# Performance work log

Hardware: AMD Instinct MI355X
Metric: run time of the kernel (lower is better)

## Reference

```python
import jax, jax.numpy as jnp
import numpy as np

N = 100_000      # total nodes across batch of graphs
E = 1_600_000    # total directed edges
D = 128          # input feature dim
H = 128          # hidden dim
OUT = 10         # output classes
B = 500          # number of graphs (200 nodes each)
L_MID = 3        # GIN layers after the first (num_layers-2)


def setup_inputs() -> dict:
    key = jax.random.key(0)
    ks = jax.random.split(key, 24)
    s = np.float32(1.0 / np.sqrt(H))
    f32 = jnp.float32
    inp = {
        'node_features': jax.random.normal(ks[0], (N, D), f32),
        'edge_src': jax.random.randint(ks[1], (E,), 0, N, jnp.int32),
        'edge_dst': jax.random.randint(ks[2], (E,), 0, N, jnp.int32),
        'graph_ids': (jnp.arange(N) // (N // B)).astype(jnp.int32),
        # GIN eps per layer (torch init: zeros)
        'eps': jnp.zeros((4,), f32),
        # pre MLP (input layer): Linear(D,H) -> BN -> ReLU -> Linear(H,H), then pre_batchnorm
        'pre_W1': jax.random.normal(ks[3], (D, H), f32) * s,
        'pre_b1': jnp.zeros((H,), f32),
        'pre_g1': jnp.ones((H,), f32),
        'pre_bt1': jnp.zeros((H,), f32),
        'pre_W2': jax.random.normal(ks[4], (H, H), f32) * s,
        'pre_b2': jnp.zeros((H,), f32),
        'pre_gout': jnp.ones((H,), f32),
        'pre_btout': jnp.zeros((H,), f32),
        # middle GIN layers (stacked over L_MID)
        'mlp_W1': jax.random.normal(ks[5], (L_MID, H, H), f32) * s,
        'mlp_b1': jnp.zeros((L_MID, H), f32),
        'mlp_g1': jnp.ones((L_MID, H), f32),
        'mlp_bt1': jnp.zeros((L_MID, H), f32),
        'mlp_W2': jax.random.normal(ks[6], (L_MID, H, H), f32) * s,
        'mlp_b2': jnp.zeros((L_MID, H), f32),
        'bn_g': jnp.ones((L_MID, H), f32),
        'bn_bt': jnp.zeros((L_MID, H), f32),
        # per-layer prediction heads
        'pred_W0': jax.random.normal(ks[7], (D, OUT), f32) * s,
        'pred_b0': jnp.zeros((OUT,), f32),
        'pred_W': jax.random.normal(ks[8], (4, H, OUT), f32) * s,
        'pred_b': jnp.zeros((4, OUT), f32),
    }
    return inp


def _mlp_bn(x, W1, b1, g1, bt1, W2, b2, go, bo):
    # MLP(num_mlp_layers=2): Linear -> BN(eval) -> ReLU -> Linear, then outer BN(eval) -> ReLU
    h = jax.nn.relu(g1 * (x @ W1 + b1) + bt1)
    h = h @ W2 + b2
    return jax.nn.relu(go * h + bo)


def reference(node_features, edge_src, edge_dst, graph_ids, eps,
              pre_W1, pre_b1, pre_g1, pre_bt1, pre_W2, pre_b2, pre_gout, pre_btout,
              mlp_W1, mlp_b1, mlp_g1, mlp_bt1, mlp_W2, mlp_b2, bn_g, bn_bt,
              pred_W0, pred_b0, pred_W, pred_b):
    def agg(h):
        # sparse Adj @ h via gather + segment_sum (sum neighbor pooling, learn_eps=True -> no self loops)
        return jax.ops.segment_sum(h[edge_src], edge_dst, num_segments=N)

    h = node_features
    reps = [h]
    pooled = agg(h) + (1.0 + eps[0]) * h
    h = _mlp_bn(pooled, pre_W1, pre_b1, pre_g1, pre_bt1, pre_W2, pre_b2, pre_gout, pre_btout)
    reps.append(h)
    for i in range(L_MID):
        pooled = agg(h) + (1.0 + eps[i + 1]) * h
        h = _mlp_bn(pooled, mlp_W1[i], mlp_b1[i], mlp_g1[i], mlp_bt1[i],
                    mlp_W2[i], mlp_b2[i], bn_g[i], bn_bt[i])
        reps.append(h)

    # graph-level sum pooling + per-layer linear heads (dropout off in eval)
    score = jax.ops.segment_sum(reps[0], graph_ids, num_segments=B) @ pred_W0 + pred_b0
    for k in range(4):
        score = score + jax.ops.segment_sum(reps[k + 1], graph_ids, num_segments=B) @ pred_W[k] + pred_b[k]
    return score  # [B, OUT]
```

## Files before the change

### kernel.cpp

```cpp
#include <hip/hip_runtime.h>
#include <hip/hip_bf16.h>

#define NN 100000
#define EE 1600000
#define HH 128
#define OUTC 10
#define BB 500
#define GSZ 200
#define LDA 136

#define NBKT 782
#define BCAP 2560
#define EPB 4096

typedef float f32x4 __attribute__((ext_vector_type(4)));
typedef __bf16 bf16x8 __attribute__((ext_vector_type(8)));

__device__ __forceinline__ float b2f(unsigned short u){
    unsigned int x = ((unsigned int)u) << 16;
    return __builtin_bit_cast(float, x);
}
__device__ __forceinline__ unsigned short f2b(float f){
    __hip_bfloat16 h = __float2bfloat16(f);
    return __builtin_bit_cast(unsigned short, h);
}

__global__ __launch_bounds__(256) void k_bucket(const int* __restrict__ src, const int* __restrict__ dst,
                                                int* __restrict__ bucket_cursor, unsigned int* __restrict__ ebuf){
    __shared__ unsigned int val[EPB];
    __shared__ unsigned short bkt[EPB];
    __shared__ int hist[NBKT];
    int t = threadIdx.x;
    int e0 = blockIdx.x * EPB;
    for (int i = t; i < NBKT; i += 256) hist[i] = 0;
    __syncthreads();
    for (int i = t; i < EPB; i += 256){
        int e = e0 + i;
        if (e < EE){
            int d = dst[e];
            int b = d >> 7;
            val[i] = ((unsigned)src[e] << 7) | (unsigned)(d & 127);
            bkt[i] = (unsigned short)b;
            atomicAdd(&hist[b], 1);
        } else {
            bkt[i] = 0xffff;
        }
    }
    __syncthreads();
    for (int i = t; i < NBKT; i += 256){
        int c = hist[i];
        hist[i] = c ? atomicAdd(&bucket_cursor[i], c) : 0;
    }
    __syncthreads();
    for (int i = t; i < EPB; i += 256){
        unsigned short b = bkt[i];
        if (b != 0xffff){
            int pos = atomicAdd(&hist[b], 1);
            if (pos < BCAP) ebuf[(int)b * BCAP + pos] = val[i];
        }
    }
}

__global__ __launch_bounds__(1024) void k_bscan(const int* __restrict__ bucket_cursor,
                                                int* __restrict__ bucket_base, int* __restrict__ row_ptr){
    __shared__ int tmp[1024];
    int t = threadIdx.x;
    int v = (t < NBKT) ? min(bucket_cursor[t], BCAP) : 0;
    tmp[t] = v; __syncthreads();
    for (int off = 1; off < 1024; off <<= 1){
        int a = (t >= off) ? tmp[t - off] : 0;
        __syncthreads();
        tmp[t] += a;
        __syncthreads();
    }
    if (t < NBKT) bucket_base[t + 1] = tmp[t];
    if (t == 0){ bucket_base[0] = 0; row_ptr[NN] = EE; }
}

__global__ __launch_bounds__(256) void k_csr(const int* __restrict__ bucket_cursor, const int* __restrict__ bucket_base,
                                             const unsigned int* __restrict__ ebuf,
                                             int* __restrict__ row_ptr, int* __restrict__ col){
    __shared__ int cnt[128];
    __shared__ int pfx[128];
    int b = blockIdx.x;
    int t = threadIdx.x;
    int c    = min(bucket_cursor[b], BCAP);
    int base = bucket_base[b];
    if (t < 128) cnt[t] = 0;
    __syncthreads();
    const unsigned int* eb = ebuf + (size_t)b * BCAP;
    for (int i = t; i < c; i += 256) atomicAdd(&cnt[eb[i] & 127], 1);
    __syncthreads();
    if (t == 0){
        int run = 0;
        for (int i = 0; i < 128; ++i){ pfx[i] = run; run += cnt[i]; }
    }
    __syncthreads();
    int node0 = b * 128;
    if (t < 128 && node0 + t < NN) row_ptr[node0 + t] = base + pfx[t];
    if (t < 128) cnt[t] = pfx[t];
    __syncthreads();
    for (int i = t; i < c; i += 256){
        unsigned int v = eb[i];
        int pos = atomicAdd(&cnt[v & 127], 1);
        col[base + pos] = (int)(v >> 7);
    }
}

__global__ __launch_bounds__(256) void k_cast(const float* __restrict__ in, unsigned short* __restrict__ out, int n){
    int i = (blockIdx.x*256 + threadIdx.x)*4;
    if (i < n){
        float4 v = *(const float4*)(in + i);
        uint2 o;
        o.x = (unsigned)f2b(v.x) | ((unsigned)f2b(v.y) << 16);
        o.y = (unsigned)f2b(v.z) | ((unsigned)f2b(v.w) << 16);
        *(uint2*)(out + i) = o;
    }
}

__global__ __launch_bounds__(256) void k_prep(const float* __restrict__ preW1, const float* __restrict__ preW2,
                                              const float* __restrict__ mlpW1, const float* __restrict__ mlpW2,
                                              unsigned short* __restrict__ Wbf){
    int idx = blockIdx.x*256 + threadIdx.x;
    int w = idx >> 14;
    int n = (idx >> 7) & 127;
    int k = idx & 127;
    const float* src;
    if      (w == 0) src = preW1;
    else if (w == 1) src = preW2;
    else if (w <  5) src = mlpW1 + (w-2)*16384;
    else             src = mlpW2 + (w-5)*16384;
    Wbf[idx] = f2b(src[k*128 + n]);
}

__device__ __forceinline__ void acc_u32(float* a, unsigned int v, int j){
    a[j]   += __builtin_bit_cast(float, v << 16);
    a[j+1] += __builtin_bit_cast(float, v & 0xffff0000u);
}
__device__ __forceinline__ void acc_u4(float* a, uint4 v){
    acc_u32(a, v.x, 0); acc_u32(a, v.y, 2); acc_u32(a, v.z, 4); acc_u32(a, v.w, 6);
}

__global__ __launch_bounds__(256) void k_agg(const int* __restrict__ row_ptr, const int* __restrict__ col,
                                             const unsigned short* __restrict__ h,
                                             const float* __restrict__ eps, int l,
                                             unsigned short* __restrict__ pooled){
    int lane = threadIdx.x & 63;
    int wv   = threadIdx.x >> 6;
    int n    = blockIdx.x*4 + wv;
    int q = lane >> 4;
    int u = lane & 15;
    int beg = row_ptr[n], end = row_ptr[n+1];
    float a[8];
    #pragma unroll
    for (int j = 0; j < 8; ++j) a[j] = 0.f;

    int e = beg;
    for (; e + 16 <= end; e += 16){
        int c0 = col[e      + q];
        int c1 = col[e + 4  + q];
        int c2 = col[e + 8  + q];
        int c3 = col[e + 12 + q];
        uint4 v0 = *(const uint4*)(h + (size_t)c0*128 + u*8);
        uint4 v1 = *(const uint4*)(h + (size_t)c1*128 + u*8);
        uint4 v2 = *(const uint4*)(h + (size_t)c2*128 + u*8);
        uint4 v3 = *(const uint4*)(h + (size_t)c3*128 + u*8);
        acc_u4(a, v0); acc_u4(a, v1); acc_u4(a, v2); acc_u4(a, v3);
    }
    for (; e + 4 <= end; e += 4){
        int c = col[e + q];
        uint4 v = *(const uint4*)(h + (size_t)c*128 + u*8);
        acc_u4(a, v);
    }
    if (e < end){
        if (e + q < end){
            int c = col[e + q];
            uint4 v = *(const uint4*)(h + (size_t)c*128 + u*8);
            acc_u4(a, v);
        }
    }
    #pragma unroll
    for (int j = 0; j < 8; ++j){
        a[j] += __shfl_xor(a[j], 16, 64);
        a[j] += __shfl_xor(a[j], 32, 64);
    }
    if (q == 0){
        float ep = 1.0f + eps[l];
        uint4 hs = *(const uint4*)(h + (size_t)n*128 + u*8);
        a[0] += ep * __builtin_bit_cast(float, hs.x << 16);
        a[1] += ep * __builtin_bit_cast(float, hs.x & 0xffff0000u);
        a[2] += ep * __builtin_bit_cast(float, hs.y << 16);
        a[3] += ep * __builtin_bit_cast(float, hs.y & 0xffff0000u);
        a[4] += ep * __builtin_bit_cast(float, hs.z << 16);
        a[5] += ep * __builtin_bit_cast(float, hs.z & 0xffff0000u);
        a[6] += ep * __builtin_bit_cast(float, hs.w << 16);
        a[7] += ep * __builtin_bit_cast(float, hs.w & 0xffff0000u);
        uint4 o;
        o.x = (unsigned)f2b(a[0]) | ((unsigned)f2b(a[1]) << 16);
        o.y = (unsigned)f2b(a[2]) | ((unsigned)f2b(a[3]) << 16);
        o.z = (unsigned)f2b(a[4]) | ((unsigned)f2b(a[5]) << 16);
        o.w = (unsigned)f2b(a[6]) | ((unsigned)f2b(a[7]) << 16);
        *(uint4*)(pooled + (size_t)n*128 + u*8) = o;
    }
}

__global__ __launch_bounds__(256) void k_mlp(const unsigned short* __restrict__ Ain,
                                             unsigned short* __restrict__ Out,
                                             const unsigned short* __restrict__ W1t,
                                             const unsigned short* __restrict__ W2t,
                                             const float* __restrict__ b1, const float* __restrict__ g1,
                                             const float* __restrict__ bt1,
                                             const float* __restrict__ b2, const float* __restrict__ g2,
                                             const float* __restrict__ bt2,
                                             float* __restrict__ Gout){
    __shared__ __align__(16) unsigned short As[64*LDA];
    __shared__ __align__(16) unsigned short Ws[128*LDA];
    int t = threadIdx.x;
    int row0 = blockIdx.x * 64;

    for (int i = t; i < 64*16; i += 256){
        int r = i >> 4, c = i & 15;
        int node = row0 + r;
        int4 v = (node < NN) ? *(const int4*)(Ain + node*128 + c*8) : make_int4(0,0,0,0);
        *(int4*)(&As[r*LDA + c*8]) = v;
    }
    for (int i = t; i < 128*16; i += 256){
        int r = i >> 4, c = i & 15;
        *(int4*)(&Ws[r*LDA + c*8]) = *(const int4*)(W1t + r*128 + c*8);
    }
    __syncthreads();

    int lane = t & 63;
    int wv = t >> 6;
    int rowbase = wv * 16;
    int m = lane & 15, q = lane >> 4;

    f32x4 acc[8];
    #pragma unroll
    for (int j = 0; j < 8; ++j) acc[j] = (f32x4){0.f,0.f,0.f,0.f};
    #pragma unroll
    for (int kk = 0; kk < 4; ++kk){
        bf16x8 a = *(const bf16x8*)(&As[(rowbase + m)*LDA + kk*32 + q*8]);
        #pragma unroll
        for (int j = 0; j < 8; ++j){
            bf16x8 b = *(const bf16x8*)(&Ws[(j*16 + m)*LDA + kk*32 + q*8]);
            acc[j] = __builtin_amdgcn_mfma_f32_16x16x32_bf16(a, b, acc[j], 0, 0, 0);
        }
    }
    #pragma unroll
    for (int j = 0; j < 8; ++j){
        int colc = j*16 + m;
        float bv = b1[colc], gv = g1[colc], btv = bt1[colc];
        #pragma unroll
        for (int r = 0; r < 4; ++r){
            float v = (acc[j][r] + bv)*gv + btv;
            v = fmaxf(v, 0.f);
            As[(rowbase + q*4 + r)*LDA + colc] = f2b(v);
        }
    }
    __syncthreads();
    for (int i = t; i < 128*16; i += 256){
        int r = i >> 4, c = i & 15;
        *(int4*)(&Ws[r*LDA + c*8]) = *(const int4*)(W2t + r*128 + c*8);
    }
    __syncthreads();

    #pragma unroll
    for (int j = 0; j < 8; ++j) acc[j] = (f32x4){0.f,0.f,0.f,0.f};
    #pragma unroll
    for (int kk = 0; kk < 4; ++kk){
        bf16x8 a = *(const bf16x8*)(&As[(rowbase + m)*LDA + kk*32 + q*8]);
        #pragma unroll
        for (int j = 0; j < 8; ++j){
            bf16x8 b = *(const bf16x8*)(&Ws[(j*16 + m)*LDA + kk*32 + q*8]);
            acc[j] = __builtin_amdgcn_mfma_f32_16x16x32_bf16(a, b, acc[j], 0, 0, 0);
        }
    }
    #pragma unroll
    for (int j = 0; j < 8; ++j){
        int colc = j*16 + m;
        float bv = b2[colc], gv = g2[colc], btv = bt2[colc];
        #pragma unroll
        for (int r = 0; r < 4; ++r){
            float v = (acc[j][r] + bv)*gv + btv;
            v = fmaxf(v, 0.f);
            As[(rowbase + q*4 + r)*LDA + colc] = f2b(v);
        }
    }
    __syncthreads();
    for (int i = t; i < 64*16; i += 256){
        int r = i >> 4, c = i & 15;
        int node = row0 + r;
        if (node < NN)
            *(int4*)(Out + node*128 + c*8) = *(const int4*)(&As[r*LDA + c*8]);
    }
    {
        int f = t & 127;
        int rbeg = (t >> 7) * 32;
        float run = 0.f;
        int curg = (row0 + rbeg) / GSZ;
        for (int r = rbeg; r < rbeg + 32; ++r){
            int node = row0 + r;
            if (node >= NN) break;
            int g = node / GSZ;
            if (g != curg){
                if (run != 0.f) atomicAdd(&Gout[curg*128 + f], run);
                run = 0.f; curg = g;
            }
            run += b2f(As[r*LDA + f]);
        }
        if (run != 0.f) atomicAdd(&Gout[curg*128 + f], run);
    }
}

__global__ __launch_bounds__(256) void k_gpool0(const float* __restrict__ h, float* __restrict__ G){
    __shared__ float r0[256], r1[256];
    int t = threadIdx.x;
    int c2 = t & 63, rg = t >> 6;
    int gb = blockIdx.x;
    const float2* h2 = (const float2*)h;
    float a0 = 0.f, a1 = 0.f;
    for (int i = rg; i < GSZ; i += 4){
        float2 v = h2[(gb*GSZ + i)*64 + c2];
        a0 += v.x; a1 += v.y;
    }
    r0[t] = a0; r1[t] = a1;
    __syncthreads();
    if (t < 64){
        float s0 = r0[t] + r0[t+64] + r0[t+128] + r0[t+192];
        float s1 = r1[t] + r1[t+64] + r1[t+128] + r1[t+192];
        float2 v; v.x = s0; v.y = s1;
        *(float2*)(G + gb*128 + t*2) = v;
    }
}

__global__ __launch_bounds__(256) void k_score(const float* __restrict__ G,
                                               const float* __restrict__ W0, const float* __restrict__ b0,
                                               const float* __restrict__ Wk, const float* __restrict__ bk,
                                               float* __restrict__ out){
    int id = blockIdx.x*256 + threadIdx.x;
    if (id >= BB*OUTC) return;
    int b = id / OUTC, o = id % OUTC;
    float s = b0[o];
    #pragma unroll
    for (int k = 0; k < 4; ++k) s += bk[k*OUTC + o];
    const float* g0 = G + b*128;
    for (int c = 0; c < 128; ++c) s += g0[c] * W0[c*OUTC + o];
    for (int k = 0; k < 4; ++k){
        const float* gk = G + (size_t)(k+1)*BB*128 + b*128;
        const float* wk = Wk + k*128*OUTC;
        for (int c = 0; c < 128; ++c) s += gk[c] * wk[c*OUTC + o];
    }
    out[id] = s;
}

extern "C" void kernel_launch(void* const* d_in, const int* in_sizes, int n_in,
                              void* d_out, int out_size, void* d_ws, size_t ws_size,
                              hipStream_t stream){
    const float* node_features = (const float*)d_in[0];
    const int*   edge_src  = (const int*)d_in[1];
    const int*   edge_dst  = (const int*)d_in[2];
    const float* eps       = (const float*)d_in[4];
    const float* pre_W1    = (const float*)d_in[5];
    const float* pre_b1    = (const float*)d_in[6];
    const float* pre_g1    = (const float*)d_in[7];
    const float* pre_bt1   = (const float*)d_in[8];
    const float* pre_W2    = (const float*)d_in[9];
    const float* pre_b2    = (const float*)d_in[10];
    const float* pre_gout  = (const float*)d_in[11];
    const float* pre_btout = (const float*)d_in[12];
    const float* mlp_W1    = (const float*)d_in[13];
    const float* mlp_b1    = (const float*)d_in[14];
    const float* mlp_g1    = (const float*)d_in[15];
    const float* mlp_bt1   = (const float*)d_in[16];
    const float* mlp_W2    = (const float*)d_in[17];
    const float* mlp_b2    = (const float*)d_in[18];
    const float* bn_g      = (const float*)d_in[19];
    const float* bn_bt     = (const float*)d_in[20];
    const float* pred_W0   = (const float*)d_in[21];
    const float* pred_b0   = (const float*)d_in[22];
    const float* pred_W    = (const float*)d_in[23];
    const float* pred_b    = (const float*)d_in[24];
    float* out = (float*)d_out;

    char* p = (char*)d_ws;
    auto alloc = [&](size_t bytes)->char*{
        char* r = p;
        p += (bytes + 255) & ~(size_t)255;
        return r;
    };
    int* bucket_cursor    = (int*)alloc((size_t)NBKT*4);
    int* bucket_base      = (int*)alloc((size_t)(NBKT+1)*4);
    int* row_ptr          = (int*)alloc((size_t)(NN+1)*4);
    int* col              = (int*)alloc((size_t)EE*4);
    unsigned int* ebuf    = (unsigned int*)alloc((size_t)NBKT*BCAP*4);
    unsigned short* Wbf   = (unsigned short*)alloc((size_t)8*128*128*2);
    unsigned short* hA    = (unsigned short*)alloc((size_t)NN*128*2);
    unsigned short* hB    = (unsigned short*)alloc((size_t)NN*128*2);
    unsigned short* pooled= (unsigned short*)alloc((size_t)NN*128*2);
    float* G              = (float*)alloc((size_t)5*BB*128*4);

    hipMemsetAsync(bucket_cursor, 0, (size_t)NBKT*4, stream);
    hipMemsetAsync(G, 0, (size_t)5*BB*128*4, stream);

    k_bucket<<<(EE + EPB - 1)/EPB, 256, 0, stream>>>(edge_src, edge_dst, bucket_cursor, ebuf);
    k_bscan<<<1, 1024, 0, stream>>>(bucket_cursor, bucket_base, row_ptr);
    k_csr<<<NBKT, 256, 0, stream>>>(bucket_cursor, bucket_base, ebuf, row_ptr, col);

    k_cast<<<(NN*128/4 + 255)/256, 256, 0, stream>>>(node_features, hA, NN*128);
    k_prep<<<512, 256, 0, stream>>>(pre_W1, pre_W2, mlp_W1, mlp_W2, Wbf);
    k_gpool0<<<BB, 256, 0, stream>>>(node_features, G);

    const unsigned short* hcur = hA;
    unsigned short* hnxt = hB;
    for (int l = 0; l < 4; ++l){
        k_agg<<<NN/4, 256, 0, stream>>>(row_ptr, col, hcur, eps, l, pooled);
        const unsigned short *W1t, *W2t;
        const float *b1,*g1,*bt1,*b2,*g2,*bt2;
        if (l == 0){
            W1t = Wbf;             W2t = Wbf + 16384;
            b1 = pre_b1; g1 = pre_g1; bt1 = pre_bt1;
            b2 = pre_b2; g2 = pre_gout; bt2 = pre_btout;
        } else {
            W1t = Wbf + (size_t)(2 + (l-1))*16384;
            W2t = Wbf + (size_t)(5 + (l-1))*16384;
            b1 = mlp_b1 + (l-1)*128; g1 = mlp_g1 + (l-1)*128; bt1 = mlp_bt1 + (l-1)*128;
            b2 = mlp_b2 + (l-1)*128; g2 = bn_g   + (l-1)*128; bt2 = bn_bt   + (l-1)*128;
        }
        k_mlp<<<(NN+63)/64, 256, 0, stream>>>(pooled, hnxt, W1t, W2t, b1,g1,bt1, b2,g2,bt2,
                                              G + (size_t)(l+1)*BB*128);
        const unsigned short* tmp = hnxt;
        hnxt = (unsigned short*)hcur;
        hcur = tmp;
    }
    k_score<<<(BB*OUTC + 255)/256, 256, 0, stream>>>(G, pred_W0, pred_b0, pred_W, pred_b, out);
}
```

Measured before the change: 629.9 us.

## Fuse neighbor aggregation into MLP kernel and merge input cast with pooling

```diff
diff --git a/kernel.cpp b/kernel.cpp
--- a/kernel.cpp
+++ b/kernel.cpp
@@ -12,6 +12,7 @@
 #define NBKT 782
 #define BCAP 2560
 #define EPB 4096
+#define NTILE 782
 
 typedef float f32x4 __attribute__((ext_vector_type(4)));
 typedef __bf16 bf16x8 __attribute__((ext_vector_type(8)));
@@ -104,17 +105,6 @@
         unsigned int v = eb[i];
         int pos = atomicAdd(&cnt[v & 127], 1);
         col[base + pos] = (int)(v >> 7);
-    }
-}
-
-__global__ __launch_bounds__(256) void k_cast(const float* __restrict__ in, unsigned short* __restrict__ out, int n){
-    int i = (blockIdx.x*256 + threadIdx.x)*4;
-    if (i < n){
-        float4 v = *(const float4*)(in + i);
-        uint2 o;
-        o.x = (unsigned)f2b(v.x) | ((unsigned)f2b(v.y) << 16);
-        o.y = (unsigned)f2b(v.z) | ((unsigned)f2b(v.w) << 16);
-        *(uint2*)(out + i) = o;
     }
 }
 
@@ -133,6 +123,31 @@
     Wbf[idx] = f2b(src[k*128 + n]);
 }
 
+__global__ __launch_bounds__(256) void k_input(const float* __restrict__ x, unsigned short* __restrict__ hA,
+                                               float* __restrict__ G){
+    __shared__ float r0[256], r1[256];
+    int t = threadIdx.x;
+    int f2 = t & 63;
+    int rg = t >> 6;
+    int g  = blockIdx.x;
+    float a0 = 0.f, a1 = 0.f;
+    for (int i = rg; i < GSZ; i += 4){
+        int node = g*GSZ + i;
+        float2 v = *(const float2*)(x + (size_t)node*128 + f2*2);
+        a0 += v.x; a1 += v.y;
+        unsigned int o = (unsigned)f2b(v.x) | ((unsigned)f2b(v.y) << 16);
+        ((unsigned int*)hA)[(size_t)node*64 + f2] = o;
+    }
+    r0[t] = a0; r1[t] = a1;
+    __syncthreads();
+    if (t < 64){
+        float s0 = r0[t] + r0[t+64] + r0[t+128] + r0[t+192];
+        float s1 = r1[t] + r1[t+64] + r1[t+128] + r1[t+192];
+        float2 v; v.x = s0; v.y = s1;
+        *(float2*)(G + g*128 + t*2) = v;
+    }
+}
+
 __device__ __forceinline__ void acc_u32(float* a, unsigned int v, int j){
     a[j]   += __builtin_bit_cast(float, v << 16);
     a[j+1] += __builtin_bit_cast(float, v & 0xffff0000u);
@@ -140,100 +155,129 @@
 __device__ __forceinline__ void acc_u4(float* a, uint4 v){
     acc_u32(a, v.x, 0); acc_u32(a, v.y, 2); acc_u32(a, v.z, 4); acc_u32(a, v.w, 6);
 }
-
-__global__ __launch_bounds__(256) void k_agg(const int* __restrict__ row_ptr, const int* __restrict__ col,
-                                             const unsigned short* __restrict__ h,
-                                             const float* __restrict__ eps, int l,
-                                             unsigned short* __restrict__ pooled){
-    int lane = threadIdx.x & 63;
-    int wv   = threadIdx.x >> 6;
-    int n    = blockIdx.x*4 + wv;
-    int q = lane >> 4;
-    int u = lane & 15;
-    int beg = row_ptr[n], end = row_ptr[n+1];
-    float a[8];
-    #pragma unroll
-    for (int j = 0; j < 8; ++j) a[j] = 0.f;
-
-    int e = beg;
-    for (; e + 16 <= end; e += 16){
-        int c0 = col[e      + q];
-        int c1 = col[e + 4  + q];
-        int c2 = col[e + 8  + q];
-        int c3 = col[e + 12 + q];
-        uint4 v0 = *(const uint4*)(h + (size_t)c0*128 + u*8);
-        uint4 v1 = *(const uint4*)(h + (size_t)c1*128 + u*8);
-        uint4 v2 = *(const uint4*)(h + (size_t)c2*128 + u*8);
-        uint4 v3 = *(const uint4*)(h + (size_t)c3*128 + u*8);
-        acc_u4(a, v0); acc_u4(a, v1); acc_u4(a, v2); acc_u4(a, v3);
-    }
-    for (; e + 4 <= end; e += 4){
-        int c = col[e + q];
-        uint4 v = *(const uint4*)(h + (size_t)c*128 + u*8);
-        acc_u4(a, v);
-    }
-    if (e < end){
-        if (e + q < end){
-            int c = col[e + q];
-            uint4 v = *(const uint4*)(h + (size_t)c*128 + u*8);
-            acc_u4(a, v);
-        }
-    }
-    #pragma unroll
-    for (int j = 0; j < 8; ++j){
-        a[j] += __shfl_xor(a[j], 16, 64);
-        a[j] += __shfl_xor(a[j], 32, 64);
-    }
-    if (q == 0){
-        float ep = 1.0f + eps[l];
-        uint4 hs = *(const uint4*)(h + (size_t)n*128 + u*8);
-        a[0] += ep * __builtin_bit_cast(float, hs.x << 16);
-        a[1] += ep * __builtin_bit_cast(float, hs.x & 0xffff0000u);
-        a[2] += ep * __builtin_bit_cast(float, hs.y << 16);
-        a[3] += ep * __builtin_bit_cast(float, hs.y & 0xffff0000u);
-        a[4] += ep * __builtin_bit_cast(float, hs.z << 16);
-        a[5] += ep * __builtin_bit_cast(float, hs.z & 0xffff0000u);
-        a[6] += ep * __builtin_bit_cast(float, hs.w << 16);
-        a[7] += ep * __builtin_bit_cast(float, hs.w & 0xffff0000u);
-        uint4 o;
-        o.x = (unsigned)f2b(a[0]) | ((unsigned)f2b(a[1]) << 16);
-        o.y = (unsigned)f2b(a[2]) | ((unsigned)f2b(a[3]) << 16);
-        o.z = (unsigned)f2b(a[4]) | ((unsigned)f2b(a[5]) << 16);
-        o.w = (unsigned)f2b(a[6]) | ((unsigned)f2b(a[7]) << 16);
-        *(uint4*)(pooled + (size_t)n*128 + u*8) = o;
-    }
-}
-
-__global__ __launch_bounds__(256) void k_mlp(const unsigned short* __restrict__ Ain,
-                                             unsigned short* __restrict__ Out,
-                                             const unsigned short* __restrict__ W1t,
-                                             const unsigned short* __restrict__ W2t,
-                                             const float* __restrict__ b1, const float* __restrict__ g1,
-                                             const float* __restrict__ bt1,
-                                             const float* __restrict__ b2, const float* __restrict__ g2,
-                                             const float* __restrict__ bt2,
-                                             float* __restrict__ Gout){
-    __shared__ __align__(16) unsigned short As[64*LDA];
+__device__ __forceinline__ void self_u4(float* a, uint4 hs, float ep){
+    a[0] += ep * __builtin_bit_cast(float, hs.x << 16);
+    a[1] += ep * __builtin_bit_cast(float, hs.x & 0xffff0000u);
+    a[2] += ep * __builtin_bit_cast(float, hs.y << 16);
+    a[3] += ep * __builtin_bit_cast(float, hs.y & 0xffff0000u);
+    a[4] += ep * __builtin_bit_cast(float, hs.z << 16);
+    a[5] += ep * __builtin_bit_cast(float, hs.z & 0xffff0000u);
+    a[6] += ep * __builtin_bit_cast(float, hs.w << 16);
+    a[7] += ep * __builtin_bit_cast(float, hs.w & 0xffff0000u);
+}
+
+__global__ __launch_bounds__(512) void k_layer(const int* __restrict__ row_ptr, const int* __restrict__ col,
+                                               const unsigned short* __restrict__ h,
+                                               const float* __restrict__ eps, int l,
+                                               unsigned short* __restrict__ Out,
+                                               const unsigned short* __restrict__ W1t,
+                                               const unsigned short* __restrict__ W2t,
+                                               const float* __restrict__ b1, const float* __restrict__ g1,
+                                               const float* __restrict__ bt1,
+                                               const float* __restrict__ b2, const float* __restrict__ g2,
+                                               const float* __restrict__ bt2,
+                                               float* __restrict__ Gout){
+    __shared__ __align__(16) unsigned short As[128*LDA];
     __shared__ __align__(16) unsigned short Ws[128*LDA];
     int t = threadIdx.x;
-    int row0 = blockIdx.x * 64;
-
-    for (int i = t; i < 64*16; i += 256){
-        int r = i >> 4, c = i & 15;
-        int node = row0 + r;
-        int4 v = (node < NN) ? *(const int4*)(Ain + node*128 + c*8) : make_int4(0,0,0,0);
-        *(int4*)(&As[r*LDA + c*8]) = v;
-    }
-    for (int i = t; i < 128*16; i += 256){
+    int lane = t & 63, wv = t >> 6;
+    int q = lane >> 4, u = lane & 15;
+    int row0 = blockIdx.x * 128;
+    float ep = 1.0f + eps[l];
+
+    for (int pi = 0; pi < 16; pi += 2){
+        int lA = wv*16 + pi, lB = lA + 1;
+        int nA = row0 + lA, nB = row0 + lB;
+        bool vA = nA < NN, vB = nB < NN;
+        float aA[8], aB[8];
+        #pragma unroll
+        for (int j = 0; j < 8; ++j){ aA[j] = 0.f; aB[j] = 0.f; }
+        int eA = 0, endA = 0, eB = 0, endB = 0;
+        uint4 hsA = make_uint4(0,0,0,0), hsB = make_uint4(0,0,0,0);
+        if (vA){ eA = row_ptr[nA]; endA = row_ptr[nA+1]; }
+        if (vB){ eB = row_ptr[nB]; endB = row_ptr[nB+1]; }
+        if (vA && q == 0) hsA = *(const uint4*)(h + (size_t)nA*128 + u*8);
+        if (vB && q == 0) hsB = *(const uint4*)(h + (size_t)nB*128 + u*8);
+
+        while (eA + 8 <= endA && eB + 8 <= endB){
+            int cA0 = col[eA + q], cA1 = col[eA + 4 + q];
+            int cB0 = col[eB + q], cB1 = col[eB + 4 + q];
+            uint4 xA0 = *(const uint4*)(h + (size_t)cA0*128 + u*8);
+            uint4 xA1 = *(const uint4*)(h + (size_t)cA1*128 + u*8);
+            uint4 xB0 = *(const uint4*)(h + (size_t)cB0*128 + u*8);
+            uint4 xB1 = *(const uint4*)(h + (size_t)cB1*128 + u*8);
+            acc_u4(aA, xA0); acc_u4(aA, xA1); acc_u4(aB, xB0); acc_u4(aB, xB1);
+            eA += 8; eB += 8;
+        }
+        while (eA + 8 <= endA){
+            int c0 = col[eA + q], c1 = col[eA + 4 + q];
+            uint4 x0 = *(const uint4*)(h + (size_t)c0*128 + u*8);
+            uint4 x1 = *(const uint4*)(h + (size_t)c1*128 + u*8);
+            acc_u4(aA, x0); acc_u4(aA, x1);
+            eA += 8;
+        }
+        while (eB + 8 <= endB){
+            int c0 = col[eB + q], c1 = col[eB + 4 + q];
+            uint4 x0 = *(const uint4*)(h + (size_t)c0*128 + u*8);
+            uint4 x1 = *(const uint4*)(h + (size_t)c1*128 + u*8);
+            acc_u4(aB, x0); acc_u4(aB, x1);
+            eB += 8;
+        }
+        while (eA + 4 <= endA){
+            int c = col[eA + q];
+            uint4 x = *(const uint4*)(h + (size_t)c*128 + u*8);
+            acc_u4(aA, x);
+            eA += 4;
+        }
+        while (eB + 4 <= endB){
+            int c = col[eB + q];
+            uint4 x = *(const uint4*)(h + (size_t)c*128 + u*8);
+            acc_u4(aB, x);
+            eB += 4;
+        }
+        if (eA + q < endA){
+            int c = col[eA + q];
+            uint4 x = *(const uint4*)(h + (size_t)c*128 + u*8);
+            acc_u4(aA, x);
+        }
+        if (eB + q < endB){
+            int c = col[eB + q];
+            uint4 x = *(const uint4*)(h + (size_t)c*128 + u*8);
+            acc_u4(aB, x);
+        }
+        #pragma unroll
+        for (int j = 0; j < 8; ++j){
+            aA[j] += __shfl_xor(aA[j], 16, 64);
+            aA[j] += __shfl_xor(aA[j], 32, 64);
+            aB[j] += __shfl_xor(aB[j], 16, 64);
+            aB[j] += __shfl_xor(aB[j], 32, 64);
+        }
+        if (q == 0){
+            self_u4(aA, hsA, ep);
+            self_u4(aB, hsB, ep);
+            uint4 oA, oB;
+            oA.x = (unsigned)f2b(aA[0]) | ((unsigned)f2b(aA[1]) << 16);
+            oA.y = (unsigned)f2b(aA[2]) | ((unsigned)f2b(aA[3]) << 16);
+            oA.z = (unsigned)f2b(aA[4]) | ((unsigned)f2b(aA[5]) << 16);
+            oA.w = (unsigned)f2b(aA[6]) | ((unsigned)f2b(aA[7]) << 16);
+            oB.x = (unsigned)f2b(aB[0]) | ((unsigned)f2b(aB[1]) << 16);
+            oB.y = (unsigned)f2b(aB[2]) | ((unsigned)f2b(aB[3]) << 16);
+            oB.z = (unsigned)f2b(aB[4]) | ((unsigned)f2b(aB[5]) << 16);
+            oB.w = (unsigned)f2b(aB[6]) | ((unsigned)f2b(aB[7]) << 16);
+            *(uint4*)(&As[lA*LDA + u*8]) = oA;
+            *(uint4*)(&As[lB*LDA + u*8]) = oB;
+        }
+    }
+    __syncthreads();
+
+    for (int i = t; i < 128*16; i += 512){
         int r = i >> 4, c = i & 15;
         *(int4*)(&Ws[r*LDA + c*8]) = *(const int4*)(W1t + r*128 + c*8);
     }
     __syncthreads();
 
-    int lane = t & 63;
-    int wv = t >> 6;
     int rowbase = wv * 16;
-    int m = lane & 15, q = lane >> 4;
+    int m = lane & 15;
 
     f32x4 acc[8];
     #pragma unroll
@@ -259,7 +303,7 @@
         }
     }
     __syncthreads();
-    for (int i = t; i < 128*16; i += 256){
+    for (int i = t; i < 128*16; i += 512){
         int r = i >> 4, c = i & 15;
         *(int4*)(&Ws[r*LDA + c*8]) = *(const int4*)(W2t + r*128 + c*8);
     }
@@ -288,7 +332,8 @@
         }
     }
     __syncthreads();
-    for (int i = t; i < 64*16; i += 256){
+
+    for (int i = t; i < 128*16; i += 512){
         int r = i >> 4, c = i & 15;
         int node = row0 + r;
         if (node < NN)
@@ -310,27 +355,6 @@
             run += b2f(As[r*LDA + f]);
         }
         if (run != 0.f) atomicAdd(&Gout[curg*128 + f], run);
-    }
-}
-
-__global__ __launch_bounds__(256) void k_gpool0(const float* __restrict__ h, float* __restrict__ G){
-    __shared__ float r0[256], r1[256];
-    int t = threadIdx.x;
-    int c2 = t & 63, rg = t >> 6;
-    int gb = blockIdx.x;
-    const float2* h2 = (const float2*)h;
-    float a0 = 0.f, a1 = 0.f;
-    for (int i = rg; i < GSZ; i += 4){
-        float2 v = h2[(gb*GSZ + i)*64 + c2];
-        a0 += v.x; a1 += v.y;
-    }
-    r0[t] = a0; r1[t] = a1;
-    __syncthreads();
-    if (t < 64){
-        float s0 = r0[t] + r0[t+64] + r0[t+128] + r0[t+192];
-        float s1 = r1[t] + r1[t+64] + r1[t+128] + r1[t+192];
-        float2 v; v.x = s0; v.y = s1;
-        *(float2*)(G + gb*128 + t*2) = v;
     }
 }
 
@@ -397,7 +421,6 @@
     unsigned short* Wbf   = (unsigned short*)alloc((size_t)8*128*128*2);
     unsigned short* hA    = (unsigned short*)alloc((size_t)NN*128*2);
     unsigned short* hB    = (unsigned short*)alloc((size_t)NN*128*2);
-    unsigned short* pooled= (unsigned short*)alloc((size_t)NN*128*2);
     float* G              = (float*)alloc((size_t)5*BB*128*4);
 
     hipMemsetAsync(bucket_cursor, 0, (size_t)NBKT*4, stream);
@@ -407,14 +430,12 @@
     k_bscan<<<1, 1024, 0, stream>>>(bucket_cursor, bucket_base, row_ptr);
     k_csr<<<NBKT, 256, 0, stream>>>(bucket_cursor, bucket_base, ebuf, row_ptr, col);
 
-    k_cast<<<(NN*128/4 + 255)/256, 256, 0, stream>>>(node_features, hA, NN*128);
+    k_input<<<BB, 256, 0, stream>>>(node_features, hA, G);
     k_prep<<<512, 256, 0, stream>>>(pre_W1, pre_W2, mlp_W1, mlp_W2, Wbf);
-    k_gpool0<<<BB, 256, 0, stream>>>(node_features, G);
 
     const unsigned short* hcur = hA;
     unsigned short* hnxt = hB;
     for (int l = 0; l < 4; ++l){
-        k_agg<<<NN/4, 256, 0, stream>>>(row_ptr, col, hcur, eps, l, pooled);
         const unsigned short *W1t, *W2t;
         const float *b1,*g1,*bt1,*b2,*g2,*bt2;
         if (l == 0){
@@ -427,8 +448,9 @@
             b1 = mlp_b1 + (l-1)*128; g1 = mlp_g1 + (l-1)*128; bt1 = mlp_bt1 + (l-1)*128;
             b2 = mlp_b2 + (l-1)*128; g2 = bn_g   + (l-1)*128; bt2 = bn_bt   + (l-1)*128;
         }
-        k_mlp<<<(NN+63)/64, 256, 0, stream>>>(pooled, hnxt, W1t, W2t, b1,g1,bt1, b2,g2,bt2,
-                                              G + (size_t)(l+1)*BB*128);
+        k_layer<<<NTILE, 512, 0, stream>>>(row_ptr, col, hcur, eps, l, hnxt, W1t, W2t,
+                                           b1,g1,bt1, b2,g2,bt2,
+                                           G + (size_t)(l+1)*BB*128);
         const unsigned short* tmp = hnxt;
         hnxt = (unsigned short*)hcur;
         hcur = tmp;
```

Result: no change. 640.2 us (+1.6%).

## Load MLP weights directly into registers and fuse input cast with graph pooling

Applied to the files above, without the earlier changes.

```diff
diff --git a/kernel.cpp b/kernel.cpp
--- a/kernel.cpp
+++ b/kernel.cpp
@@ -104,17 +104,6 @@
         unsigned int v = eb[i];
         int pos = atomicAdd(&cnt[v & 127], 1);
         col[base + pos] = (int)(v >> 7);
-    }
-}
-
-__global__ __launch_bounds__(256) void k_cast(const float* __restrict__ in, unsigned short* __restrict__ out, int n){
-    int i = (blockIdx.x*256 + threadIdx.x)*4;
-    if (i < n){
-        float4 v = *(const float4*)(in + i);
-        uint2 o;
-        o.x = (unsigned)f2b(v.x) | ((unsigned)f2b(v.y) << 16);
-        o.y = (unsigned)f2b(v.z) | ((unsigned)f2b(v.w) << 16);
-        *(uint2*)(out + i) = o;
     }
 }
 
@@ -131,6 +120,35 @@
     else if (w <  5) src = mlpW1 + (w-2)*16384;
     else             src = mlpW2 + (w-5)*16384;
     Wbf[idx] = f2b(src[k*128 + n]);
+}
+
+__global__ __launch_bounds__(256) void k_input(const float* __restrict__ x, unsigned short* __restrict__ hA,
+                                               float* __restrict__ G){
+    __shared__ float r0[256], r1[256];
+    int t = threadIdx.x;
+    int f2 = t & 63;
+    int rg = t >> 6;
+    int g  = blockIdx.x;
+    if (t < 128){
+        #pragma unroll
+        for (int k = 1; k < 5; ++k) G[(size_t)k*BB*128 + g*128 + t] = 0.f;
+    }
+    float a0 = 0.f, a1 = 0.f;
+    for (int i = rg; i < GSZ; i += 4){
+        int node = g*GSZ + i;
+        float2 v = *(const float2*)(x + (size_t)node*128 + f2*2);
+        a0 += v.x; a1 += v.y;
+        unsigned int o = (unsigned)f2b(v.x) | ((unsigned)f2b(v.y) << 16);
+        ((unsigned int*)hA)[(size_t)node*64 + f2] = o;
+    }
+    r0[t] = a0; r1[t] = a1;
+    __syncthreads();
+    if (t < 64){
+        float s0 = r0[t] + r0[t+64] + r0[t+128] + r0[t+192];
+        float s1 = r1[t] + r1[t+64] + r1[t+128] + r1[t+192];
+        float2 v; v.x = s0; v.y = s1;
+        *(float2*)(G + g*128 + t*2) = v;
+    }
 }
 
 __device__ __forceinline__ void acc_u32(float* a, unsigned int v, int j){
@@ -214,7 +232,6 @@
                                              const float* __restrict__ bt2,
                                              float* __restrict__ Gout){
     __shared__ __align__(16) unsigned short As[64*LDA];
-    __shared__ __align__(16) unsigned short Ws[128*LDA];
     int t = threadIdx.x;
     int row0 = blockIdx.x * 64;
 
@@ -224,10 +241,6 @@
         int4 v = (node < NN) ? *(const int4*)(Ain + node*128 + c*8) : make_int4(0,0,0,0);
         *(int4*)(&As[r*LDA + c*8]) = v;
     }
-    for (int i = t; i < 128*16; i += 256){
-        int r = i >> 4, c = i & 15;
-        *(int4*)(&Ws[r*LDA + c*8]) = *(const int4*)(W1t + r*128 + c*8);
-    }
     __syncthreads();
 
     int lane = t & 63;
@@ -236,17 +249,29 @@
     int m = lane & 15, q = lane >> 4;
 
     f32x4 acc[8];
+    bf16x8 bcur[8], bnxt[8];
     #pragma unroll
     for (int j = 0; j < 8; ++j) acc[j] = (f32x4){0.f,0.f,0.f,0.f};
     #pragma unroll
+    for (int j = 0; j < 8; ++j) bcur[j] = *(const bf16x8*)(W1t + (j*16 + m)*128 + q*8);
+    #pragma unroll
     for (int kk = 0; kk < 4; ++kk){
+        if (kk < 3){
+            #pragma unroll
+            for (int j = 0; j < 8; ++j)
+                bnxt[j] = *(const bf16x8*)(W1t + (j*16 + m)*128 + (kk+1)*32 + q*8);
+        }
         bf16x8 a = *(const bf16x8*)(&As[(rowbase + m)*LDA + kk*32 + q*8]);
         #pragma unroll
-        for (int j = 0; j < 8; ++j){
-            bf16x8 b = *(const bf16x8*)(&Ws[(j*16 + m)*LDA + kk*32 + q*8]);
-            acc[j] = __builtin_amdgcn_mfma_f32_16x16x32_bf16(a, b, acc[j], 0, 0, 0);
-        }
-    }
+        for (int j = 0; j < 8; ++j)
+            acc[j] = __builtin_amdgcn_mfma_f32_16x16x32_bf16(a, bcur[j], acc[j], 0, 0, 0);
+        if (kk < 3){
+            #pragma unroll
+            for (int j = 0; j < 8; ++j) bcur[j] = bnxt[j];
+        }
+    }
+    #pragma unroll
+    for (int j = 0; j < 8; ++j) bcur[j] = *(const bf16x8*)(W2t + (j*16 + m)*128 + q*8);
     #pragma unroll
     for (int j = 0; j < 8; ++j){
         int colc = j*16 + m;
@@ -258,22 +283,23 @@
             As[(rowbase + q*4 + r)*LDA + colc] = f2b(v);
         }
     }
-    __syncthreads();
-    for (int i = t; i < 128*16; i += 256){
-        int r = i >> 4, c = i & 15;
-        *(int4*)(&Ws[r*LDA + c*8]) = *(const int4*)(W2t + r*128 + c*8);
-    }
-    __syncthreads();
 
     #pragma unroll
     for (int j = 0; j < 8; ++j) acc[j] = (f32x4){0.f,0.f,0.f,0.f};
     #pragma unroll
     for (int kk = 0; kk < 4; ++kk){
+        if (kk < 3){
+            #pragma unroll
+            for (int j = 0; j < 8; ++j)
+                bnxt[j] = *(const bf16x8*)(W2t + (j*16 + m)*128 + (kk+1)*32 + q*8);
+        }
         bf16x8 a = *(const bf16x8*)(&As[(rowbase + m)*LDA + kk*32 + q*8]);
         #pragma unroll
-        for (int j = 0; j < 8; ++j){
-            bf16x8 b = *(const bf16x8*)(&Ws[(j*16 + m)*LDA + kk*32 + q*8]);
-            acc[j] = __builtin_amdgcn_mfma_f32_16x16x32_bf16(a, b, acc[j], 0, 0, 0);
+        for (int j = 0; j < 8; ++j)
+            acc[j] = __builtin_amdgcn_mfma_f32_16x16x32_bf16(a, bcur[j], acc[j], 0, 0, 0);
+        if (kk < 3){
+            #pragma unroll
+            for (int j = 0; j < 8; ++j) bcur[j] = bnxt[j];
         }
     }
     #pragma unroll
@@ -288,6 +314,7 @@
         }
     }
     __syncthreads();
+
     for (int i = t; i < 64*16; i += 256){
         int r = i >> 4, c = i & 15;
         int node = row0 + r;
@@ -310,27 +337,6 @@
             run += b2f(As[r*LDA + f]);
         }
         if (run != 0.f) atomicAdd(&Gout[curg*128 + f], run);
-    }
-}
-
-__global__ __launch_bounds__(256) void k_gpool0(const float* __restrict__ h, float* __restrict__ G){
-    __shared__ float r0[256], r1[256];
-    int t = threadIdx.x;
-    int c2 = t & 63, rg = t >> 6;
-    int gb = blockIdx.x;
-    const float2* h2 = (const float2*)h;
-    float a0 = 0.f, a1 = 0.f;
-    for (int i = rg; i < GSZ; i += 4){
-        float2 v = h2[(gb*GSZ + i)*64 + c2];
-        a0 += v.x; a1 += v.y;
-    }
-    r0[t] = a0; r1[t] = a1;
-    __syncthreads();
-    if (t < 64){
-        float s0 = r0[t] + r0[t+64] + r0[t+128] + r0[t+192];
-        float s1 = r1[t] + r1[t+64] + r1[t+128] + r1[t+192];
-        float2 v; v.x = s0; v.y = s1;
-        *(float2*)(G + gb*128 + t*2) = v;
     }
 }
 
@@ -401,15 +407,13 @@
     float* G              = (float*)alloc((size_t)5*BB*128*4);
 
     hipMemsetAsync(bucket_cursor, 0, (size_t)NBKT*4, stream);
-    hipMemsetAsync(G, 0, (size_t)5*BB*128*4, stream);
 
     k_bucket<<<(EE + EPB - 1)/EPB, 256, 0, stream>>>(edge_src, edge_dst, bucket_cursor, ebuf);
     k_bscan<<<1, 1024, 0, stream>>>(bucket_cursor, bucket_base, row_ptr);
     k_csr<<<NBKT, 256, 0, stream>>>(bucket_cursor, bucket_base, ebuf, row_ptr, col);
 
-    k_cast<<<(NN*128/4 + 255)/256, 256, 0, stream>>>(node_features, hA, NN*128);
+    k_input<<<BB, 256, 0, stream>>>(node_features, hA, G);
     k_prep<<<512, 256, 0, stream>>>(pre_W1, pre_W2, mlp_W1, mlp_W2, Wbf);
-    k_gpool0<<<BB, 256, 0, stream>>>(node_features, G);
 
     const unsigned short* hcur = hA;
     unsigned short* hnxt = hB;
```

After: 732.0 us. +16.2%, slower.
